# Kernel optimization log

Hardware: AMD Instinct MI355X
Metric: run time of the kernel (lower is better)

Reference implementation:

```python
import jax, jax.numpy as jnp
import numpy as np

N_NODES = 102400
N_EDGES = 1638400
NUM_GRAPHS = 128
IN_DIM = 128
HID = 128
OUT_DIM = 2
NUM_LAYERS = 3
BN_EPS = 1e-5


def setup_inputs() -> dict:
    key = jax.random.key(0)
    ks = jax.random.split(key, 12)
    x = jax.random.normal(ks[0], (N_NODES, IN_DIM), dtype=jnp.float32)
    edge_index = jax.random.randint(ks[1], (2, N_EDGES), 0, N_NODES, dtype=jnp.int64)
    # 128 graphs of 800 nodes each, sorted segment ids
    batch = jnp.repeat(jnp.arange(NUM_GRAPHS, dtype=jnp.int64), N_NODES // NUM_GRAPHS)
    s = 1.0 / np.sqrt(HID)
    W_conv = jax.random.uniform(ks[2], (NUM_LAYERS, HID, HID), jnp.float32, -s, s)
    b_conv = jnp.zeros((NUM_LAYERS, HID), jnp.float32)
    gamma = jnp.ones((NUM_LAYERS, HID), jnp.float32)
    beta = jnp.zeros((NUM_LAYERS, HID), jnp.float32)
    s2 = 1.0 / np.sqrt(3 * HID)
    W_mp1 = jax.random.uniform(ks[3], (3 * HID, 3 * HID), jnp.float32, -s2, s2)
    b_mp1 = jax.random.uniform(ks[4], (3 * HID,), jnp.float32, -s2, s2)
    W_mp2 = jax.random.uniform(ks[5], (3 * HID, OUT_DIM), jnp.float32, -s2, s2)
    b_mp2 = jax.random.uniform(ks[6], (OUT_DIM,), jnp.float32, -s2, s2)
    return {"x": x, "edge_index": edge_index, "batch": batch,
            "W_conv": W_conv, "b_conv": b_conv, "gamma": gamma, "beta": beta,
            "W_mp1": W_mp1, "b_mp1": b_mp1, "W_mp2": W_mp2, "b_mp2": b_mp2}


def _gcn_norm(edge_index, n):
    # add self loops, symmetric normalization: norm_e = deg^-1/2[src] * deg^-1/2[dst]
    loop = jnp.arange(n, dtype=edge_index.dtype)
    src = jnp.concatenate([edge_index[0], loop])
    dst = jnp.concatenate([edge_index[1], loop])
    deg = jax.ops.segment_sum(jnp.ones_like(dst, dtype=jnp.float32), dst, num_segments=n)
    dinv = jnp.where(deg > 0, jax.lax.rsqrt(deg), 0.0)
    return src, dst, dinv[src] * dinv[dst]


def reference(x, edge_index, batch, W_conv, b_conv, gamma, beta, W_mp1, b_mp1, W_mp2, b_mp2):
    n = x.shape[0]
    src, dst, norm = _gcn_norm(edge_index, n)
    for i in range(NUM_LAYERS):
        h = x @ W_conv[i]                                    # [N, HID]
        h = jax.ops.segment_sum(h[src] * norm[:, None], dst, num_segments=n) + b_conv[i]
        h = jax.nn.relu(h)
        mu = jnp.mean(h, axis=0)
        var = jnp.var(h, axis=0)                             # biased, as torch BN
        x = (h - mu) * jax.lax.rsqrt(var + BN_EPS) * gamma[i] + beta[i]
        # dropout p=0.0 -> no-op
    # readout: max pool, mean pool, first-node gather
    x1 = jax.ops.segment_max(x, batch, num_segments=NUM_GRAPHS)
    cnt = jax.ops.segment_sum(jnp.ones((n,), jnp.float32), batch, num_segments=NUM_GRAPHS)
    x2 = jax.ops.segment_sum(x, batch, num_segments=NUM_GRAPHS) / cnt[:, None]
    first_idx = jnp.searchsorted(batch, jnp.arange(NUM_GRAPHS, dtype=batch.dtype))
    x3 = x[first_idx]
    g = jnp.concatenate([x1, x2, x3], axis=1)                # [B, 3*HID]
    g = (g @ W_mp1 + b_mp1) @ W_mp2 + b_mp2
    return jax.nn.log_softmax(g, axis=1)
```

## Files before the change

kernel.cpp:

```cpp
#include <hip/hip_runtime.h>
#include <hip/hip_bf16.h>
#include <cstdint>

#define N_NODESC  102400
#define N_EDGESC  1638400
#define NUM_GRAPHS 128
#define NPG       800
#define HID       128
#define BN_EPS    1e-5f

typedef short short8 __attribute__((ext_vector_type(8)));
typedef float f32x4  __attribute__((ext_vector_type(4)));

__device__ __forceinline__ unsigned short f2bf(float f){
    union { __hip_bfloat16 h; unsigned short u; } cv;
    cv.h = __float2bfloat16(f);
    return cv.u;
}
__device__ __forceinline__ float bflo(unsigned int g){ return __uint_as_float(g << 16); }
__device__ __forceinline__ float bfhi(unsigned int g){ return __uint_as_float(g & 0xffff0000u); }
__device__ __forceinline__ float bfu(unsigned short u){ return __uint_as_float(((unsigned int)u) << 16); }

__global__ void k_count(const int* __restrict__ ei, int* __restrict__ deg){
    int e = blockIdx.x*blockDim.x + threadIdx.x;
    if (e < N_EDGESC) atomicAdd(&deg[ei[N_EDGESC + e]], 1);
}

__global__ __launch_bounds__(1024) void k_scan_a(const int* __restrict__ deg, int* __restrict__ row_ptr,
                                                 float* __restrict__ dinv, int* __restrict__ chunkTot){
    __shared__ int sh[1024];
    int t = threadIdx.x;
    int i = blockIdx.x*1024 + t;
    int v = deg[i];
    dinv[i] = rsqrtf((float)(v + 1));
    sh[t] = v;
    __syncthreads();
    for (int off = 1; off < 1024; off <<= 1){
        int add = (t >= off) ? sh[t - off] : 0;
        __syncthreads();
        sh[t] += add;
        __syncthreads();
    }
    row_ptr[i] = sh[t] - v;
    if (t == 1023) chunkTot[blockIdx.x] = sh[t];
}

__global__ __launch_bounds__(128) void k_scan_b(const int* __restrict__ chunkTot, int* __restrict__ chunkOff,
                                                int* __restrict__ row_ptr){
    __shared__ int sh[128];
    int t = threadIdx.x;
    int v = (t < 100) ? chunkTot[t] : 0;
    sh[t] = v;
    __syncthreads();
    for (int off = 1; off < 128; off <<= 1){
        int add = (t >= off) ? sh[t - off] : 0;
        __syncthreads();
        sh[t] += add;
        __syncthreads();
    }
    if (t < 100) chunkOff[t] = sh[t] - v;
    if (t == 0)  row_ptr[N_NODESC] = N_EDGESC;
}

__global__ __launch_bounds__(1024) void k_scan_c(int* __restrict__ row_ptr, const int* __restrict__ chunkOff){
    int i = blockIdx.x*1024 + threadIdx.x;
    row_ptr[i] += chunkOff[blockIdx.x];
}

__global__ void k_scatter(const int* __restrict__ ei, const int* __restrict__ row_ptr,
                          int* __restrict__ cursor, const float* __restrict__ dinv,
                          int* __restrict__ srcS, float* __restrict__ normS){
    int e = blockIdx.x*blockDim.x + threadIdx.x;
    if (e < N_EDGESC){
        int s = ei[e];
        int d = ei[N_EDGESC + e];
        int pos = row_ptr[d] + atomicAdd(&cursor[d], 1);
        srcS[pos]  = s;
        normS[pos] = dinv[s] * dinv[d];
    }
}

__global__ __launch_bounds__(256) void k_prepw0(const float* __restrict__ W, unsigned short* __restrict__ Wt){
    int idx = blockIdx.x*256 + threadIdx.x;
    int n = idx & 127, k = idx >> 7;
    Wt[n*128 + k] = f2bf(W[k*128 + n]);
}

template<int F32IN>
__global__ __launch_bounds__(256) void k_gemm_mfma(const void* __restrict__ Xin,
        const unsigned short* __restrict__ Wt, const float* __restrict__ biasv,
        unsigned short* __restrict__ H){
    int l   = threadIdx.x & 63;
    int wid = threadIdx.x >> 6;
    int R   = blockIdx.x*64 + wid*16;
    int r0  = l & 15;
    int kg  = l >> 4;
    short8 a[4];
    if (F32IN){
        const float* X = (const float*)Xin;
        #pragma unroll
        for (int kk = 0; kk < 4; kk++){
            const float* p = X + (size_t)(R + r0)*HID + kk*32 + kg*8;
            float4 u = *(const float4*)p;
            float4 v = *(const float4*)(p + 4);
            short8 t;
            t[0]=(short)f2bf(u.x); t[1]=(short)f2bf(u.y); t[2]=(short)f2bf(u.z); t[3]=(short)f2bf(u.w);
            t[4]=(short)f2bf(v.x); t[5]=(short)f2bf(v.y); t[6]=(short)f2bf(v.z); t[7]=(short)f2bf(v.w);
            a[kk] = t;
        }
    } else {
        const unsigned short* X = (const unsigned short*)Xin;
        #pragma unroll
        for (int kk = 0; kk < 4; kk++)
            a[kk] = *(const short8*)(X + (size_t)(R + r0)*HID + kk*32 + kg*8);
    }
    f32x4 acc[8];
    #pragma unroll
    for (int i = 0; i < 8; i++) acc[i] = (f32x4)(0.f);
    #pragma unroll
    for (int kk = 0; kk < 4; kk++){
        #pragma unroll
        for (int nf = 0; nf < 8; nf++){
            short8 b = *(const short8*)(Wt + (size_t)(nf*16 + r0)*HID + kk*32 + kg*8);
            acc[nf] = __builtin_amdgcn_mfma_f32_16x16x32_bf16(a[kk], b, acc[nf], 0, 0, 0);
        }
    }
    #pragma unroll
    for (int nf = 0; nf < 8; nf++){
        float bv = biasv[nf*16 + r0];
        #pragma unroll
        for (int r = 0; r < 4; r++){
            int row = R + kg*4 + r;
            H[(size_t)row*HID + nf*16 + r0] = f2bf(acc[nf][r] + bv);
        }
    }
}

__global__ __launch_bounds__(256) void k_agg(const unsigned int* __restrict__ Hb, const int* __restrict__ row_ptr,
                                             const int* __restrict__ srcS, const float* __restrict__ normS,
                                             const float* __restrict__ dinv, const float* __restrict__ bconv,
                                             unsigned int* __restrict__ OUT, float* __restrict__ sum,
                                             float* __restrict__ sumsq){
    int lane = threadIdx.x & 63;
    int w    = threadIdx.x >> 6;
    int wave = blockIdx.x*4 + w;
    int nw   = gridDim.x*4;
    float2 bc = ((const float2*)bconv)[lane];
    float sx0 = 0.f, sx1 = 0.f, sq0 = 0.f, sq1 = 0.f;
    for (int n = wave; n < N_NODESC; n += nw){
        int e0 = row_ptr[n], e1 = row_ptr[n+1];
        float ax = 0.f, ay = 0.f;
        int e = e0;
        while (e < e1 && (e & 3)){
            int s = srcS[e]; float nv = normS[e];
            unsigned int g = Hb[(size_t)s*64 + lane];
            ax = fmaf(nv, bflo(g), ax); ay = fmaf(nv, bfhi(g), ay);
            e++;
        }
        for (; e + 8 <= e1; e += 8){
            int4   sa = *(const int4*)(srcS + e);
            int4   sb = *(const int4*)(srcS + e + 4);
            float4 na = *(const float4*)(normS + e);
            float4 nb = *(const float4*)(normS + e + 4);
            unsigned int g0 = Hb[(size_t)sa.x*64 + lane];
            unsigned int g1 = Hb[(size_t)sa.y*64 + lane];
            unsigned int g2 = Hb[(size_t)sa.z*64 + lane];
            unsigned int g3 = Hb[(size_t)sa.w*64 + lane];
            unsigned int g4 = Hb[(size_t)sb.x*64 + lane];
            unsigned int g5 = Hb[(size_t)sb.y*64 + lane];
            unsigned int g6 = Hb[(size_t)sb.z*64 + lane];
            unsigned int g7 = Hb[(size_t)sb.w*64 + lane];
            ax = fmaf(na.x, bflo(g0), ax); ay = fmaf(na.x, bfhi(g0), ay);
            ax = fmaf(na.y, bflo(g1), ax); ay = fmaf(na.y, bfhi(g1), ay);
            ax = fmaf(na.z, bflo(g2), ax); ay = fmaf(na.z, bfhi(g2), ay);
            ax = fmaf(na.w, bflo(g3), ax); ay = fmaf(na.w, bfhi(g3), ay);
            ax = fmaf(nb.x, bflo(g4), ax); ay = fmaf(nb.x, bfhi(g4), ay);
            ax = fmaf(nb.y, bflo(g5), ax); ay = fmaf(nb.y, bfhi(g5), ay);
            ax = fmaf(nb.z, bflo(g6), ax); ay = fmaf(nb.z, bfhi(g6), ay);
            ax = fmaf(nb.w, bflo(g7), ax); ay = fmaf(nb.w, bfhi(g7), ay);
        }
        if (e + 4 <= e1){
            int4   sa = *(const int4*)(srcS + e);
            float4 na = *(const float4*)(normS + e);
            unsigned int g0 = Hb[(size_t)sa.x*64 + lane];
            unsigned int g1 = Hb[(size_t)sa.y*64 + lane];
            unsigned int g2 = Hb[(size_t)sa.z*64 + lane];
            unsigned int g3 = Hb[(size_t)sa.w*64 + lane];
            ax = fmaf(na.x, bflo(g0), ax); ay = fmaf(na.x, bfhi(g0), ay);
            ax = fmaf(na.y, bflo(g1), ax); ay = fmaf(na.y, bfhi(g1), ay);
            ax = fmaf(na.z, bflo(g2), ax); ay = fmaf(na.z, bfhi(g2), ay);
            ax = fmaf(na.w, bflo(g3), ax); ay = fmaf(na.w, bfhi(g3), ay);
            e += 4;
        }
        for (; e < e1; e++){
            int s = srcS[e]; float nv = normS[e];
            unsigned int g = Hb[(size_t)s*64 + lane];
            ax = fmaf(nv, bflo(g), ax); ay = fmaf(nv, bfhi(g), ay);
        }
        float di = dinv[n]; float ws = di*di;
        unsigned int gn = Hb[(size_t)n*64 + lane];
        ax = fmaf(ws, bflo(gn), ax); ay = fmaf(ws, bfhi(gn), ay);
        ax = fmaxf(ax + bc.x, 0.f); ay = fmaxf(ay + bc.y, 0.f);
        unsigned int o = ((unsigned int)f2bf(ay) << 16) | (unsigned int)f2bf(ax);
        __builtin_nontemporal_store(o, &OUT[(size_t)n*64 + lane]);
        sx0 += ax; sq0 = fmaf(ax, ax, sq0);
        sx1 += ay; sq1 = fmaf(ay, ay, sq1);
    }
    __shared__ float shs[4][128];
    __shared__ float shq[4][128];
    shs[w][2*lane]   = sx0; shs[w][2*lane+1] = sx1;
    shq[w][2*lane]   = sq0; shq[w][2*lane+1] = sq1;
    __syncthreads();
    int t = threadIdx.x;
    if (t < 128){
        atomicAdd(&sum[t],   shs[0][t] + shs[1][t] + shs[2][t] + shs[3][t]);
        atomicAdd(&sumsq[t], shq[0][t] + shq[1][t] + shq[2][t] + shq[3][t]);
    }
}

__global__ __launch_bounds__(128) void k_finalize(const float* __restrict__ sum, const float* __restrict__ sumsq,
                                                  const float* __restrict__ gamma, const float* __restrict__ beta,
                                                  const float* __restrict__ Wnext, float* __restrict__ A,
                                                  float* __restrict__ B, unsigned short* __restrict__ WpT,
                                                  float* __restrict__ biasv, int hasNext){
    __shared__ float Ash[128], Bsh[128];
    int c = threadIdx.x;
    const float invN = 1.0f / (float)N_NODESC;
    float mu  = sum[c] * invN;
    float var = sumsq[c] * invN - mu*mu;
    float is  = rsqrtf(var + BN_EPS);
    float a = is * gamma[c];
    float b = beta[c] - mu * a;
    A[c] = a; B[c] = b; Ash[c] = a; Bsh[c] = b;
    __syncthreads();
    if (hasNext){
        float bv = 0.f;
        for (int k = 0; k < 128; k++){
            float w = Wnext[k*128 + c];
            WpT[c*128 + k] = f2bf(Ash[k] * w);
            bv = fmaf(Bsh[k], w, bv);
        }
        biasv[c] = bv;
    }
}

__global__ __launch_bounds__(1024) void k_pool(const unsigned short* __restrict__ X, const float* __restrict__ A,
                                               const float* __restrict__ B, float* __restrict__ g){
    __shared__ float shm[8][128];
    __shared__ float shs[8][128];
    int t = threadIdx.x;
    int c = t & 127, sl = t >> 7;
    int gr = blockIdx.x;
    float a = A[c], b = B[c];
    const unsigned short* base = X + ((size_t)gr*NPG + sl*100)*HID;
    float mx = -1e30f, sm = 0.f;
    for (int i = 0; i < 100; i++){
        float v = fmaf(bfu(base[(size_t)i*HID + c]), a, b);
        mx = fmaxf(mx, v); sm += v;
    }
    shm[sl][c] = mx; shs[sl][c] = sm;
    if (sl == 0) g[gr*384 + 256 + c] = fmaf(bfu(base[c]), a, b);
    __syncthreads();
    if (t < 128){
        float m = shm[0][t], s = shs[0][t];
        #pragma unroll
        for (int q = 1; q < 8; q++){ m = fmaxf(m, shm[q][t]); s += shs[q][t]; }
        g[gr*384 + t]       = m;
        g[gr*384 + 128 + t] = s * (1.0f/(float)NPG);
    }
}

__global__ __launch_bounds__(512) void k_mlp(const float* __restrict__ g, const float* __restrict__ W1,
                                             const float* __restrict__ b1, const float* __restrict__ W2,
                                             const float* __restrict__ b2, float* __restrict__ out){
    __shared__ float row[384];
    __shared__ float t1[384];
    __shared__ float r0[512], r1[512];
    int t = threadIdx.x, gr = blockIdx.x;
    if (t < 384) row[t] = g[gr*384 + t];
    __syncthreads();
    if (t < 384){
        float acc = b1[t];
        for (int k = 0; k < 384; k++) acc = fmaf(row[k], W1[(size_t)k*384 + t], acc);
        t1[t] = acc;
    }
    __syncthreads();
    float p0 = 0.f, p1 = 0.f;
    if (t < 384){ float v = t1[t]; p0 = v*W2[t*2]; p1 = v*W2[t*2+1]; }
    r0[t] = p0; r1[t] = p1; __syncthreads();
    for (int off = 256; off > 0; off >>= 1){
        if (t < off){ r0[t] += r0[t+off]; r1[t] += r1[t+off]; }
        __syncthreads();
    }
    if (t == 0){
        float o0 = r0[0] + b2[0], o1 = r1[0] + b2[1];
        float m = fmaxf(o0, o1);
        float lse = m + logf(expf(o0 - m) + expf(o1 - m));
        out[gr*2 + 0] = o0 - lse;
        out[gr*2 + 1] = o1 - lse;
    }
}

extern "C" void kernel_launch(void* const* d_in, const int* in_sizes, int n_in,
                              void* d_out, int out_size, void* d_ws, size_t ws_size,
                              hipStream_t stream){
    const float* x     = (const float*)d_in[0];
    const int*   ei    = (const int*)d_in[1];
    const float* Wconv = (const float*)d_in[3];
    const float* bconv = (const float*)d_in[4];
    const float* gamma = (const float*)d_in[5];
    const float* beta  = (const float*)d_in[6];
    const float* W1    = (const float*)d_in[7];
    const float* b1    = (const float*)d_in[8];
    const float* W2    = (const float*)d_in[9];
    const float* b2    = (const float*)d_in[10];
    float* out = (float*)d_out;

    char* p = (char*)d_ws;
    size_t off = 0;
    auto alloc = [&](size_t bytes)->char* {
        char* r = p + off; off += (bytes + 255) & ~(size_t)255; return r;
    };
    unsigned short* buf1 = (unsigned short*)alloc((size_t)N_NODESC*HID*2);
    unsigned short* buf2 = (unsigned short*)alloc((size_t)N_NODESC*HID*2);
    int*   srcS    = (int*)  alloc((size_t)N_EDGESC*4);
    float* normS   = (float*)alloc((size_t)N_EDGESC*4);
    int*   row_ptr = (int*)  alloc((size_t)(N_NODESC+1)*4);
    int*   deg     = (int*)  alloc((size_t)N_NODESC*4);
    float* dinv    = (float*)alloc((size_t)N_NODESC*4);
    int*   chunkTot= (int*)  alloc(512);
    int*   chunkOff= (int*)  alloc(512);
    float* stats   = (float*)alloc(3*2*128*4);
    float* AB      = (float*)alloc(3*2*128*4);
    unsigned short* Wt0 = (unsigned short*)alloc(128*128*2);
    unsigned short* WpT = (unsigned short*)alloc(128*128*2);
    float* biasv   = (float*)alloc(512);
    float* g       = (float*)alloc((size_t)NUM_GRAPHS*384*4);
    (void)ws_size; (void)in_sizes; (void)n_in; (void)out_size;

    hipMemsetAsync(deg,   0, (size_t)N_NODESC*4, stream);
    hipMemsetAsync(stats, 0, 3*2*128*4, stream);
    hipMemsetAsync(biasv, 0, 512, stream);

    k_count  <<<(N_EDGESC+255)/256, 256, 0, stream>>>(ei, deg);
    k_scan_a <<<N_NODESC/1024, 1024, 0, stream>>>(deg, row_ptr, dinv, chunkTot);
    k_scan_b <<<1, 128, 0, stream>>>(chunkTot, chunkOff, row_ptr);
    k_scan_c <<<N_NODESC/1024, 1024, 0, stream>>>(row_ptr, chunkOff);
    hipMemsetAsync(deg, 0, (size_t)N_NODESC*4, stream);
    k_scatter<<<(N_EDGESC+255)/256, 256, 0, stream>>>(ei, row_ptr, deg, dinv, srcS, normS);
    k_prepw0 <<<64, 256, 0, stream>>>(Wconv, Wt0);

    for (int l = 0; l < 3; l++){
        if (l == 0)
            k_gemm_mfma<1><<<N_NODESC/64, 256, 0, stream>>>((const void*)x, Wt0, biasv, buf1);
        else
            k_gemm_mfma<0><<<N_NODESC/64, 256, 0, stream>>>((const void*)buf2, WpT, biasv, buf1);
        k_agg<<<2048, 256, 0, stream>>>((const unsigned int*)buf1, row_ptr, srcS, normS, dinv,
                                        bconv + l*HID, (unsigned int*)buf2,
                                        stats + l*256, stats + l*256 + 128);
        k_finalize<<<1, 128, 0, stream>>>(stats + l*256, stats + l*256 + 128,
                                          gamma + l*HID, beta + l*HID,
                                          Wconv + (size_t)(l+1 < 3 ? l+1 : 0)*HID*HID,
                                          AB + l*256, AB + l*256 + 128,
                                          WpT, biasv, (l < 2) ? 1 : 0);
    }
    k_pool<<<NUM_GRAPHS, 1024, 0, stream>>>(buf2, AB + 2*256, AB + 2*256 + 128, g);
    k_mlp <<<NUM_GRAPHS, 512, 0, stream>>>(g, W1, b1, W2, b2, out);
}
```

Baseline: 647.1 us.

## Fold symmetric GCN norm into GEMM epilogue and aggregate two edges per wave

The per-edge norm array is removed. The source-side dinv is folded into the GEMM epilogue (H scaled by dinv[row]) and the destination-side dinv is applied once per node after aggregation, so the gather loop becomes a plain sum. The aggregation now has each half-wave process a different edge with 8-byte loads and combines the halves with a cross-lane shuffle. A zero padding row is added so the self-loop or odd edge can be handled without branches. This cuts the per-edge norm reads and scatter writes and gives each wave twice as many gathers in flight. The cost is bf16 rounding of the scaled H, plus a shuffle and a half-idle wave during the epilogue.

Result: slower. 670.0 us (+3.5%).

```diff
diff --git a/kernel.cpp b/kernel.cpp
--- a/kernel.cpp
+++ b/kernel.cpp
@@ -68,15 +68,13 @@
 }
 
 __global__ void k_scatter(const int* __restrict__ ei, const int* __restrict__ row_ptr,
-                          int* __restrict__ cursor, const float* __restrict__ dinv,
-                          int* __restrict__ srcS, float* __restrict__ normS){
+                          int* __restrict__ cursor, int* __restrict__ srcS){
     int e = blockIdx.x*blockDim.x + threadIdx.x;
     if (e < N_EDGESC){
         int s = ei[e];
         int d = ei[N_EDGESC + e];
         int pos = row_ptr[d] + atomicAdd(&cursor[d], 1);
-        srcS[pos]  = s;
-        normS[pos] = dinv[s] * dinv[d];
+        srcS[pos] = s;
     }
 }
 
@@ -89,7 +87,7 @@
 template<int F32IN>
 __global__ __launch_bounds__(256) void k_gemm_mfma(const void* __restrict__ Xin,
         const unsigned short* __restrict__ Wt, const float* __restrict__ biasv,
-        unsigned short* __restrict__ H){
+        const float* __restrict__ dinv, unsigned short* __restrict__ H){
     int l   = threadIdx.x & 63;
     int wid = threadIdx.x >> 6;
     int R   = blockIdx.x*64 + wid*16;
@@ -125,91 +123,88 @@
             acc[nf] = __builtin_amdgcn_mfma_f32_16x16x32_bf16(a[kk], b, acc[nf], 0, 0, 0);
         }
     }
+    float bv[8];
     #pragma unroll
-    for (int nf = 0; nf < 8; nf++){
-        float bv = biasv[nf*16 + r0];
-        #pragma unroll
-        for (int r = 0; r < 4; r++){
-            int row = R + kg*4 + r;
-            H[(size_t)row*HID + nf*16 + r0] = f2bf(acc[nf][r] + bv);
-        }
-    }
-}
-
-__global__ __launch_bounds__(256) void k_agg(const unsigned int* __restrict__ Hb, const int* __restrict__ row_ptr,
-                                             const int* __restrict__ srcS, const float* __restrict__ normS,
-                                             const float* __restrict__ dinv, const float* __restrict__ bconv,
-                                             unsigned int* __restrict__ OUT, float* __restrict__ sum,
+    for (int nf = 0; nf < 8; nf++) bv[nf] = biasv[nf*16 + r0];
+    #pragma unroll
+    for (int r = 0; r < 4; r++){
+        int row = R + kg*4 + r;
+        float di = dinv[row];
+        #pragma unroll
+        for (int nf = 0; nf < 8; nf++)
+            H[(size_t)row*HID + nf*16 + r0] = f2bf(di * (acc[nf][r] + bv[nf]));
+    }
+}
+
+__global__ __launch_bounds__(256) void k_agg(const uint2* __restrict__ Hb2, const int* __restrict__ row_ptr,
+                                             const int* __restrict__ srcS, const float* __restrict__ dinv,
+                                             const float* __restrict__ bconv,
+                                             uint2* __restrict__ OUT2, float* __restrict__ sum,
                                              float* __restrict__ sumsq){
     int lane = threadIdx.x & 63;
+    int half = lane >> 5;
+    int lc   = lane & 31;
     int w    = threadIdx.x >> 6;
     int wave = blockIdx.x*4 + w;
     int nw   = gridDim.x*4;
-    float2 bc = ((const float2*)bconv)[lane];
-    float sx0 = 0.f, sx1 = 0.f, sq0 = 0.f, sq1 = 0.f;
+    float4 bc = ((const float4*)bconv)[lc];
+    float sx0=0,sx1=0,sx2=0,sx3=0,sq0=0,sq1=0,sq2=0,sq3=0;
     for (int n = wave; n < N_NODESC; n += nw){
         int e0 = row_ptr[n], e1 = row_ptr[n+1];
-        float ax = 0.f, ay = 0.f;
+        float a0=0,a1=0,a2=0,a3=0;
         int e = e0;
-        while (e < e1 && (e & 3)){
-            int s = srcS[e]; float nv = normS[e];
-            unsigned int g = Hb[(size_t)s*64 + lane];
-            ax = fmaf(nv, bflo(g), ax); ay = fmaf(nv, bfhi(g), ay);
-            e++;
-        }
         for (; e + 8 <= e1; e += 8){
-            int4   sa = *(const int4*)(srcS + e);
-            int4   sb = *(const int4*)(srcS + e + 4);
-            float4 na = *(const float4*)(normS + e);
-            float4 nb = *(const float4*)(normS + e + 4);
-            unsigned int g0 = Hb[(size_t)sa.x*64 + lane];
-            unsigned int g1 = Hb[(size_t)sa.y*64 + lane];
-            unsigned int g2 = Hb[(size_t)sa.z*64 + lane];
-            unsigned int g3 = Hb[(size_t)sa.w*64 + lane];
-            unsigned int g4 = Hb[(size_t)sb.x*64 + lane];
-            unsigned int g5 = Hb[(size_t)sb.y*64 + lane];
-            unsigned int g6 = Hb[(size_t)sb.z*64 + lane];
-            unsigned int g7 = Hb[(size_t)sb.w*64 + lane];
-            ax = fmaf(na.x, bflo(g0), ax); ay = fmaf(na.x, bfhi(g0), ay);
-            ax = fmaf(na.y, bflo(g1), ax); ay = fmaf(na.y, bfhi(g1), ay);
-            ax = fmaf(na.z, bflo(g2), ax); ay = fmaf(na.z, bfhi(g2), ay);
-            ax = fmaf(na.w, bflo(g3), ax); ay = fmaf(na.w, bfhi(g3), ay);
-            ax = fmaf(nb.x, bflo(g4), ax); ay = fmaf(nb.x, bfhi(g4), ay);
-            ax = fmaf(nb.y, bflo(g5), ax); ay = fmaf(nb.y, bfhi(g5), ay);
-            ax = fmaf(nb.z, bflo(g6), ax); ay = fmaf(nb.z, bfhi(g6), ay);
-            ax = fmaf(nb.w, bflo(g7), ax); ay = fmaf(nb.w, bfhi(g7), ay);
-        }
-        if (e + 4 <= e1){
-            int4   sa = *(const int4*)(srcS + e);
-            float4 na = *(const float4*)(normS + e);
-            unsigned int g0 = Hb[(size_t)sa.x*64 + lane];
-            unsigned int g1 = Hb[(size_t)sa.y*64 + lane];
-            unsigned int g2 = Hb[(size_t)sa.z*64 + lane];
-            unsigned int g3 = Hb[(size_t)sa.w*64 + lane];
-            ax = fmaf(na.x, bflo(g0), ax); ay = fmaf(na.x, bfhi(g0), ay);
-            ax = fmaf(na.y, bflo(g1), ax); ay = fmaf(na.y, bfhi(g1), ay);
-            ax = fmaf(na.z, bflo(g2), ax); ay = fmaf(na.z, bfhi(g2), ay);
-            ax = fmaf(na.w, bflo(g3), ax); ay = fmaf(na.w, bfhi(g3), ay);
-            e += 4;
-        }
-        for (; e < e1; e++){
-            int s = srcS[e]; float nv = normS[e];
-            unsigned int g = Hb[(size_t)s*64 + lane];
-            ax = fmaf(nv, bflo(g), ax); ay = fmaf(nv, bfhi(g), ay);
-        }
-        float di = dinv[n]; float ws = di*di;
-        unsigned int gn = Hb[(size_t)n*64 + lane];
-        ax = fmaf(ws, bflo(gn), ax); ay = fmaf(ws, bfhi(gn), ay);
-        ax = fmaxf(ax + bc.x, 0.f); ay = fmaxf(ay + bc.y, 0.f);
-        unsigned int o = ((unsigned int)f2bf(ay) << 16) | (unsigned int)f2bf(ax);
-        __builtin_nontemporal_store(o, &OUT[(size_t)n*64 + lane]);
-        sx0 += ax; sq0 = fmaf(ax, ax, sq0);
-        sx1 += ay; sq1 = fmaf(ay, ay, sq1);
+            int s0 = srcS[e     + half];
+            int s1 = srcS[e + 2 + half];
+            int s2 = srcS[e + 4 + half];
+            int s3 = srcS[e + 6 + half];
+            uint2 g0 = Hb2[(size_t)s0*32 + lc];
+            uint2 g1 = Hb2[(size_t)s1*32 + lc];
+            uint2 g2 = Hb2[(size_t)s2*32 + lc];
+            uint2 g3 = Hb2[(size_t)s3*32 + lc];
+            a0 += bflo(g0.x); a1 += bfhi(g0.x); a2 += bflo(g0.y); a3 += bfhi(g0.y);
+            a0 += bflo(g1.x); a1 += bfhi(g1.x); a2 += bflo(g1.y); a3 += bfhi(g1.y);
+            a0 += bflo(g2.x); a1 += bfhi(g2.x); a2 += bflo(g2.y); a3 += bfhi(g2.y);
+            a0 += bflo(g3.x); a1 += bfhi(g3.x); a2 += bflo(g3.y); a3 += bfhi(g3.y);
+        }
+        for (; e + 2 <= e1; e += 2){
+            int s = srcS[e + half];
+            uint2 g = Hb2[(size_t)s*32 + lc];
+            a0 += bflo(g.x); a1 += bfhi(g.x); a2 += bflo(g.y); a3 += bfhi(g.y);
+        }
+        {
+            int s;
+            if (e < e1) s = half ? n : srcS[e];
+            else        s = half ? N_NODESC : n;
+            uint2 g = Hb2[(size_t)s*32 + lc];
+            a0 += bflo(g.x); a1 += bfhi(g.x); a2 += bflo(g.y); a3 += bfhi(g.y);
+        }
+        a0 += __shfl_xor(a0, 32);
+        a1 += __shfl_xor(a1, 32);
+        a2 += __shfl_xor(a2, 32);
+        a3 += __shfl_xor(a3, 32);
+        if (half == 0){
+            float dn = dinv[n];
+            a0 = fmaxf(fmaf(a0, dn, bc.x), 0.f);
+            a1 = fmaxf(fmaf(a1, dn, bc.y), 0.f);
+            a2 = fmaxf(fmaf(a2, dn, bc.z), 0.f);
+            a3 = fmaxf(fmaf(a3, dn, bc.w), 0.f);
+            uint2 o;
+            o.x = ((unsigned int)f2bf(a1) << 16) | (unsigned int)f2bf(a0);
+            o.y = ((unsigned int)f2bf(a3) << 16) | (unsigned int)f2bf(a2);
+            OUT2[(size_t)n*32 + lc] = o;
+            sx0 += a0; sq0 = fmaf(a0,a0,sq0);
+            sx1 += a1; sq1 = fmaf(a1,a1,sq1);
+            sx2 += a2; sq2 = fmaf(a2,a2,sq2);
+            sx3 += a3; sq3 = fmaf(a3,a3,sq3);
+        }
     }
     __shared__ float shs[4][128];
     __shared__ float shq[4][128];
-    shs[w][2*lane]   = sx0; shs[w][2*lane+1] = sx1;
-    shq[w][2*lane]   = sq0; shq[w][2*lane+1] = sq1;
+    if (half == 0){
+        shs[w][4*lc+0] = sx0; shs[w][4*lc+1] = sx1; shs[w][4*lc+2] = sx2; shs[w][4*lc+3] = sx3;
+        shq[w][4*lc+0] = sq0; shq[w][4*lc+1] = sq1; shq[w][4*lc+2] = sq2; shq[w][4*lc+3] = sq3;
+    }
     __syncthreads();
     int t = threadIdx.x;
     if (t < 128){
@@ -321,10 +316,9 @@
     auto alloc = [&](size_t bytes)->char* {
         char* r = p + off; off += (bytes + 255) & ~(size_t)255; return r;
     };
-    unsigned short* buf1 = (unsigned short*)alloc((size_t)N_NODESC*HID*2);
+    unsigned short* buf1 = (unsigned short*)alloc((size_t)(N_NODESC+1)*HID*2);
     unsigned short* buf2 = (unsigned short*)alloc((size_t)N_NODESC*HID*2);
     int*   srcS    = (int*)  alloc((size_t)N_EDGESC*4);
-    float* normS   = (float*)alloc((size_t)N_EDGESC*4);
     int*   row_ptr = (int*)  alloc((size_t)(N_NODESC+1)*4);
     int*   deg     = (int*)  alloc((size_t)N_NODESC*4);
     float* dinv    = (float*)alloc((size_t)N_NODESC*4);
@@ -341,22 +335,23 @@
     hipMemsetAsync(deg,   0, (size_t)N_NODESC*4, stream);
     hipMemsetAsync(stats, 0, 3*2*128*4, stream);
     hipMemsetAsync(biasv, 0, 512, stream);
+    hipMemsetAsync(buf1 + (size_t)N_NODESC*HID, 0, HID*2, stream);
 
     k_count  <<<(N_EDGESC+255)/256, 256, 0, stream>>>(ei, deg);
     k_scan_a <<<N_NODESC/1024, 1024, 0, stream>>>(deg, row_ptr, dinv, chunkTot);
     k_scan_b <<<1, 128, 0, stream>>>(chunkTot, chunkOff, row_ptr);
     k_scan_c <<<N_NODESC/1024, 1024, 0, stream>>>(row_ptr, chunkOff);
     hipMemsetAsync(deg, 0, (size_t)N_NODESC*4, stream);
-    k_scatter<<<(N_EDGESC+255)/256, 256, 0, stream>>>(ei, row_ptr, deg, dinv, srcS, normS);
+    k_scatter<<<(N_EDGESC+255)/256, 256, 0, stream>>>(ei, row_ptr, deg, srcS);
     k_prepw0 <<<64, 256, 0, stream>>>(Wconv, Wt0);
 
     for (int l = 0; l < 3; l++){
         if (l == 0)
-            k_gemm_mfma<1><<<N_NODESC/64, 256, 0, stream>>>((const void*)x, Wt0, biasv, buf1);
+            k_gemm_mfma<1><<<N_NODESC/64, 256, 0, stream>>>((const void*)x, Wt0, biasv, dinv, buf1);
         else
-            k_gemm_mfma<0><<<N_NODESC/64, 256, 0, stream>>>((const void*)buf2, WpT, biasv, buf1);
-        k_agg<<<2048, 256, 0, stream>>>((const unsigned int*)buf1, row_ptr, srcS, normS, dinv,
-                                        bconv + l*HID, (unsigned int*)buf2,
+            k_gemm_mfma<0><<<N_NODESC/64, 256, 0, stream>>>((const void*)buf2, WpT, biasv, dinv, buf1);
+        k_agg<<<2048, 256, 0, stream>>>((const uint2*)buf1, row_ptr, srcS, dinv,
+                                        bconv + l*HID, (uint2*)buf2,
                                         stats + l*256, stats + l*256 + 128);
         k_finalize<<<1, 128, 0, stream>>>(stats + l*256, stats + l*256 + 128,
                                           gamma + l*HID, beta + l*HID,
```

## Partition degree count and CSR scatter by node range; parallelize weight folding

Applied to the files above, without the earlier changes.

The count and scatter kernels now launch 8x as many blocks. Each block handles only edges whose destination falls in one of eight node-range partitions, so the atomics and scattered writes for a block land in a region that fits in L2. The single-block finalize kernel is split in two: a small kernel computes the BN affine terms and the folded bias, and a 64-block kernel writes the scaled, transposed bf16 weights in parallel. The trade-off is reading the destination indices eight times and issuing one extra launch per layer.

New measurement: 689.6 us. 1.07x slower.

```diff
diff --git a/kernel.cpp b/kernel.cpp
--- a/kernel.cpp
+++ b/kernel.cpp
@@ -8,6 +8,7 @@
 #define NPG       800
 #define HID       128
 #define BN_EPS    1e-5f
+#define NPR       12800
 
 typedef short short8 __attribute__((ext_vector_type(8)));
 typedef float f32x4  __attribute__((ext_vector_type(4)));
@@ -21,9 +22,13 @@
 __device__ __forceinline__ float bfhi(unsigned int g){ return __uint_as_float(g & 0xffff0000u); }
 __device__ __forceinline__ float bfu(unsigned short u){ return __uint_as_float(((unsigned int)u) << 16); }
 
-__global__ void k_count(const int* __restrict__ ei, int* __restrict__ deg){
-    int e = blockIdx.x*blockDim.x + threadIdx.x;
-    if (e < N_EDGESC) atomicAdd(&deg[ei[N_EDGESC + e]], 1);
+__global__ __launch_bounds__(256) void k_count(const int* __restrict__ ei, int* __restrict__ deg){
+    int b = blockIdx.x;
+    int r = b & 7;
+    int e = (b >> 3)*256 + threadIdx.x;
+    int lo = r * NPR;
+    int d = __builtin_nontemporal_load(&ei[N_EDGESC + e]);
+    if (d >= lo && d < lo + NPR) atomicAdd(&deg[d], 1);
 }
 
 __global__ __launch_bounds__(1024) void k_scan_a(const int* __restrict__ deg, int* __restrict__ row_ptr,
@@ -67,13 +72,16 @@
     row_ptr[i] += chunkOff[blockIdx.x];
 }
 
-__global__ void k_scatter(const int* __restrict__ ei, const int* __restrict__ row_ptr,
-                          int* __restrict__ cursor, const float* __restrict__ dinv,
-                          int* __restrict__ srcS, float* __restrict__ normS){
-    int e = blockIdx.x*blockDim.x + threadIdx.x;
-    if (e < N_EDGESC){
+__global__ __launch_bounds__(256) void k_scatter(const int* __restrict__ ei, const int* __restrict__ row_ptr,
+                                                 int* __restrict__ cursor, const float* __restrict__ dinv,
+                                                 int* __restrict__ srcS, float* __restrict__ normS){
+    int b = blockIdx.x;
+    int r = b & 7;
+    int e = (b >> 3)*256 + threadIdx.x;
+    int lo = r * NPR;
+    int d = __builtin_nontemporal_load(&ei[N_EDGESC + e]);
+    if (d >= lo && d < lo + NPR){
         int s = ei[e];
-        int d = ei[N_EDGESC + e];
         int pos = row_ptr[d] + atomicAdd(&cursor[d], 1);
         srcS[pos]  = s;
         normS[pos] = dinv[s] * dinv[d];
@@ -218,12 +226,11 @@
     }
 }
 
-__global__ __launch_bounds__(128) void k_finalize(const float* __restrict__ sum, const float* __restrict__ sumsq,
-                                                  const float* __restrict__ gamma, const float* __restrict__ beta,
-                                                  const float* __restrict__ Wnext, float* __restrict__ A,
-                                                  float* __restrict__ B, unsigned short* __restrict__ WpT,
-                                                  float* __restrict__ biasv, int hasNext){
-    __shared__ float Ash[128], Bsh[128];
+__global__ __launch_bounds__(128) void k_fin1(const float* __restrict__ sum, const float* __restrict__ sumsq,
+                                              const float* __restrict__ gamma, const float* __restrict__ beta,
+                                              const float* __restrict__ Wnext, float* __restrict__ A,
+                                              float* __restrict__ B, float* __restrict__ biasv, int hasNext){
+    __shared__ float Bsh[128];
     int c = threadIdx.x;
     const float invN = 1.0f / (float)N_NODESC;
     float mu  = sum[c] * invN;
@@ -231,17 +238,21 @@
     float is  = rsqrtf(var + BN_EPS);
     float a = is * gamma[c];
     float b = beta[c] - mu * a;
-    A[c] = a; B[c] = b; Ash[c] = a; Bsh[c] = b;
+    A[c] = a; B[c] = b; Bsh[c] = b;
     __syncthreads();
     if (hasNext){
         float bv = 0.f;
-        for (int k = 0; k < 128; k++){
-            float w = Wnext[k*128 + c];
-            WpT[c*128 + k] = f2bf(Ash[k] * w);
-            bv = fmaf(Bsh[k], w, bv);
-        }
+        for (int k = 0; k < 128; k++)
+            bv = fmaf(Bsh[k], Wnext[k*128 + c], bv);
         biasv[c] = bv;
     }
+}
+
+__global__ __launch_bounds__(256) void k_fin2(const float* __restrict__ A, const float* __restrict__ Wnext,
+                                              unsigned short* __restrict__ WpT){
+    int idx = blockIdx.x*256 + threadIdx.x;
+    int c = idx >> 7, k = idx & 127;
+    WpT[c*128 + k] = f2bf(A[k] * Wnext[k*128 + c]);
 }
 
 __global__ __launch_bounds__(1024) void k_pool(const unsigned short* __restrict__ X, const float* __restrict__ A,
@@ -342,12 +353,12 @@
     hipMemsetAsync(stats, 0, 3*2*128*4, stream);
     hipMemsetAsync(biasv, 0, 512, stream);
 
-    k_count  <<<(N_EDGESC+255)/256, 256, 0, stream>>>(ei, deg);
+    k_count  <<<(N_EDGESC/256)*8, 256, 0, stream>>>(ei, deg);
     k_scan_a <<<N_NODESC/1024, 1024, 0, stream>>>(deg, row_ptr, dinv, chunkTot);
     k_scan_b <<<1, 128, 0, stream>>>(chunkTot, chunkOff, row_ptr);
     k_scan_c <<<N_NODESC/1024, 1024, 0, stream>>>(row_ptr, chunkOff);
     hipMemsetAsync(deg, 0, (size_t)N_NODESC*4, stream);
-    k_scatter<<<(N_EDGESC+255)/256, 256, 0, stream>>>(ei, row_ptr, deg, dinv, srcS, normS);
+    k_scatter<<<(N_EDGESC/256)*8, 256, 0, stream>>>(ei, row_ptr, deg, dinv, srcS, normS);
     k_prepw0 <<<64, 256, 0, stream>>>(Wconv, Wt0);
 
     for (int l = 0; l < 3; l++){
@@ -358,11 +369,14 @@
         k_agg<<<2048, 256, 0, stream>>>((const unsigned int*)buf1, row_ptr, srcS, normS, dinv,
                                         bconv + l*HID, (unsigned int*)buf2,
                                         stats + l*256, stats + l*256 + 128);
-        k_finalize<<<1, 128, 0, stream>>>(stats + l*256, stats + l*256 + 128,
-                                          gamma + l*HID, beta + l*HID,
-                                          Wconv + (size_t)(l+1 < 3 ? l+1 : 0)*HID*HID,
-                                          AB + l*256, AB + l*256 + 128,
-                                          WpT, biasv, (l < 2) ? 1 : 0);
+        k_fin1<<<1, 128, 0, stream>>>(stats + l*256, stats + l*256 + 128,
+                                      gamma + l*HID, beta + l*HID,
+                                      Wconv + (size_t)(l+1 < 3 ? l+1 : 0)*HID*HID,
+                                      AB + l*256, AB + l*256 + 128,
+                                      biasv, (l < 2) ? 1 : 0);
+        if (l < 2)
+            k_fin2<<<64, 256, 0, stream>>>(AB + l*256,
+                                           Wconv + (size_t)(l+1)*HID*HID, WpT);
     }
     k_pool<<<NUM_GRAPHS, 1024, 0, stream>>>(buf2, AB + 2*256, AB + 2*256 + 128, g);
     k_mlp <<<NUM_GRAPHS, 512, 0, stream>>>(g, W1, b1, W2, b2, out);
```
